# Kernel optimization log

Measured on AMD Instinct MI355X. Metric: run time of the kernel, lower is better.

## Reference

```python
import jax, jax.numpy as jnp
import numpy as np


def _gru(xs, w_ih, w_hh, b_ih, b_hh):
    """Batch-first torch-style GRU. xs: (B,T,I) -> (B,T,H)."""
    b, t, _ = xs.shape
    H = w_hh.shape[1]
    xp = xs @ w_ih.T + b_ih  # (B,T,3H): precomputed input projections

    def step(h, xp_t):
        gh = h @ w_hh.T + b_hh  # (B,3H)
        xr, xz, xn = xp_t[:, :H], xp_t[:, H:2 * H], xp_t[:, 2 * H:]
        hr, hz, hn = gh[:, :H], gh[:, H:2 * H], gh[:, 2 * H:]
        r = jax.nn.sigmoid(xr + hr)
        z = jax.nn.sigmoid(xz + hz)
        n = jnp.tanh(xn + r * hn)
        h_new = (1.0 - z) * n + z * h
        return h_new, h_new

    h0 = jnp.zeros((b, H), dtype=xs.dtype)
    _, hs = jax.lax.scan(step, h0, jnp.swapaxes(xp, 0, 1))  # (T,B,H)
    return jnp.swapaxes(hs, 0, 1)


def reference(x, gru_w_ih, gru_w_hh, gru_b_ih, gru_b_hh, filter_alpha, pc_w, pc_b, pat_re, pat_im):
    b, t, _ = x.shape
    xs = x[..., 0]  # (B,T)
    # quaternionic lift: (w,x,y,z) = (s, .1s, .01s, .001s)
    quat = jnp.stack([xs, 0.1 * xs, 0.01 * xs, 0.001 * xs], axis=-1)  # (B,T,4)
    evolved = _gru(quat, gru_w_ih, gru_w_hh, gru_b_ih, gru_b_hh)  # (B,T,4*dim)
    dim2 = evolved.shape[-1] // 2
    ev = evolved.reshape(b, t, dim2, 2)
    ec = jax.lax.complex(ev[..., 0], ev[..., 1])  # (B,T,2*dim) complex64
    fd = jnp.fft.fft(ec, axis=1)
    kmag = jnp.abs(fd) + 1e-10
    pf = filter_alpha[0] * jnp.arctan(jnp.log(kmag))  # phase filter
    filtered = fd * jax.lax.complex(jnp.cos(pf), jnp.sin(pf))
    ft = jnp.fft.ifft(filtered, axis=1).real  # (B,T,2*dim) float32
    coh = ft.reshape(b, t, -1) @ pc_w.T + pc_b  # (B,T,dim)
    # interference logits: |<x_t, pattern_j>|^2, computed only for batch 0
    # (faithful to original; x_t is real so vdot conjugation is a no-op)
    x0 = coh[0]  # (T,dim)
    zr = x0 @ pat_re.T  # (T,V)
    zi = x0 @ pat_im.T  # (T,V)
    logits0 = zr * zr + zi * zi
    return logits0[None]  # (1,T,V)


def setup_inputs() -> dict:
    key = jax.random.key(0)
    ks = jax.random.split(key, 10)
    dim, T, V = 128, 4096, 32000
    H = dim * 4
    return {
        "x": jax.random.normal(ks[0], (1, T, 1), jnp.float32),
        "gru_w_ih": jax.random.normal(ks[1], (3 * H, 4), jnp.float32) * 0.05,
        "gru_w_hh": jax.random.normal(ks[2], (3 * H, H), jnp.float32) * 0.05,
        "gru_b_ih": jax.random.normal(ks[3], (3 * H,), jnp.float32) * 0.05,
        "gru_b_hh": jax.random.normal(ks[4], (3 * H,), jnp.float32) * 0.05,
        "filter_alpha": jnp.ones((1,), jnp.float32) * 1.5,
        "pc_w": jax.random.normal(ks[5], (dim, 2 * dim), jnp.float32) * 0.05,
        "pc_b": jax.random.normal(ks[6], (dim,), jnp.float32) * 0.05,
        "pat_re": jax.random.normal(ks[7], (V, dim), jnp.float32) * 0.1,
        "pat_im": jax.random.normal(ks[8], (V, dim), jnp.float32) * 0.1,
    }
```

## Files before the change

kernel.cpp:

```cpp
#include <hip/hip_runtime.h>

#define T_STEPS 4096
#define HID     512
#define NCH     256
#define DIM     128
#define VOCAB   32000
#define GRU_WGS 16

__device__ __forceinline__ float fast_sigmoid(float x) {
  x = fminf(fmaxf(x, -30.f), 30.f);
  const float e = __expf(-x);
  return __fdividef(1.f, 1.f + e);
}
__device__ __forceinline__ float fast_tanh(float x) {
  x = fminf(fmaxf(x, -15.f), 15.f);
  const float e = __expf(2.f * x);
  return __fdividef(e - 1.f, e + 1.f);
}

template <int CTRL>
__device__ __forceinline__ float dpp_add(float v) {
  const int s = __builtin_amdgcn_update_dpp(0, __float_as_int(v), CTRL, 0xF, 0xF, true);
  return v + __int_as_float(s);
}
__device__ __forceinline__ float red16(float v) {
  v = dpp_add<0xB1>(v);
  v = dpp_add<0x4E>(v);
  v = dpp_add<0x124>(v);
  v = dpp_add<0x128>(v);
  return v;
}

__global__ __launch_bounds__(512) void gru_kernel(
    const float* __restrict__ x,
    const float* __restrict__ w_ih,
    const float* __restrict__ w_hh,
    const float* __restrict__ b_ih,
    const float* __restrict__ b_hh,
    unsigned long long* hg,
    float* __restrict__ evolved)
{
  __shared__ float hs[HID];
  __shared__ float xl[T_STEPS];
  const int tid  = threadIdx.x;
  const int wave = tid >> 6;
  const int lane = tid & 63;
  const int team = lane >> 4;
  const int p    = lane & 15;
  const int pr   = p & 7;
  const int j    = blockIdx.x * 32 + wave * 4 + team;
  const int k0   = p * 32;

  {
    const float4* x4 = reinterpret_cast<const float4*>(x);
    float4* xl4 = reinterpret_cast<float4*>(xl);
    for (int u = tid; u < T_STEPS / 4; u += 512) xl4[u] = x4[u];
  }

  float4 w[3][8];
#pragma unroll
  for (int d = 0; d < 3; ++d) {
    const float4* wr = reinterpret_cast<const float4*>(w_hh + (size_t)(d * HID + j) * HID);
#pragma unroll
    for (int qq = 0; qq < 8; ++qq) {
      const int r = (qq + pr) & 7;
      w[d][qq] = wr[p * 8 + r];
    }
  }
  float c3[3], bi3[3], bh3[3];
#pragma unroll
  for (int d = 0; d < 3; ++d) {
    int r = d * HID + j;
    c3[d]  = w_ih[r*4+0] + 0.1f*w_ih[r*4+1] + 0.01f*w_ih[r*4+2] + 0.001f*w_ih[r*4+3];
    bi3[d] = b_ih[r];
    bh3[d] = b_hh[r];
  }
  __syncthreads();

  float hprev = 0.0f;
  for (int s = 1; s <= T_STEPS; ++s) {
    const int rb = (s - 1) & 1;
    const int wb = s & 1;
    const unsigned int want = (unsigned int)(s - 1);
    const unsigned long long* rs = hg + rb * HID;

    const float xt = xl[s - 1];

    unsigned long long v =
        __hip_atomic_load(rs + tid, __ATOMIC_RELAXED, __HIP_MEMORY_SCOPE_AGENT);
    for (;;) {
      hs[tid] = __uint_as_float((unsigned int)v);
      const unsigned long long nv =
          __hip_atomic_load(rs + tid, __ATOMIC_RELAXED, __HIP_MEMORY_SCOPE_AGENT);
      if (__syncthreads_and((unsigned int)(v >> 32) == want)) break;
      v = nv;
    }

    float a0 = 0.f, a1 = 0.f, a2 = 0.f;
#pragma unroll
    for (int qq = 0; qq < 8; ++qq) {
      const int r = (qq + pr) & 7;
      const float4 h4 = *reinterpret_cast<const float4*>(&hs[k0 + 4 * r]);
      a0 = fmaf(w[0][qq].x, h4.x, a0);
      a0 = fmaf(w[0][qq].y, h4.y, a0);
      a0 = fmaf(w[0][qq].z, h4.z, a0);
      a0 = fmaf(w[0][qq].w, h4.w, a0);
      a1 = fmaf(w[1][qq].x, h4.x, a1);
      a1 = fmaf(w[1][qq].y, h4.y, a1);
      a1 = fmaf(w[1][qq].z, h4.z, a1);
      a1 = fmaf(w[1][qq].w, h4.w, a1);
      a2 = fmaf(w[2][qq].x, h4.x, a2);
      a2 = fmaf(w[2][qq].y, h4.y, a2);
      a2 = fmaf(w[2][qq].z, h4.z, a2);
      a2 = fmaf(w[2][qq].w, h4.w, a2);
    }

    a0 = red16(a0); a1 = red16(a1); a2 = red16(a2);

    if (p == 0) {
      const float rg = fast_sigmoid(fmaf(xt, c3[0], bi3[0]) + a0 + bh3[0]);
      const float zg = fast_sigmoid(fmaf(xt, c3[1], bi3[1]) + a1 + bh3[1]);
      const float ng = fast_tanh(fmaf(xt, c3[2], bi3[2]) + rg * (a2 + bh3[2]));
      const float hn = (1.0f - zg) * ng + zg * hprev;
      hprev = hn;
      const unsigned long long pk =
          ((unsigned long long)(unsigned int)s << 32) | (unsigned long long)__float_as_uint(hn);
      __hip_atomic_store(hg + wb * HID + j, pk, __ATOMIC_RELAXED, __HIP_MEMORY_SCOPE_AGENT);
      evolved[(size_t)(s - 1) * HID + j] = hn;
    }
  }
}

__device__ __forceinline__ void fft4096(float2* buf, const float2* tw, int tid)
{
  for (int st = 0; st < 12; ++st) {
    const int half = 1 << st;
    const int sh = 11 - st;
    for (int i = tid; i < 2048; i += 256) {
      const int blk = i >> st;
      const int pos = i & (half - 1);
      const int idx = blk * (2 << st) + pos;
      const float2 t = tw[pos << sh];
      const float2 u = buf[idx];
      const float2 v = buf[idx + half];
      const float tr = v.x * t.x - v.y * t.y;
      const float ti = v.x * t.y + v.y * t.x;
      buf[idx]        = make_float2(u.x + tr, u.y + ti);
      buf[idx + half] = make_float2(u.x - tr, u.y - ti);
    }
    __syncthreads();
  }
}

__global__ __launch_bounds__(256) void fft_kernel(
    const float* __restrict__ evolved,
    const float* __restrict__ alpha_p,
    float* __restrict__ ft)
{
  __shared__ float2 buf[4096];
  __shared__ float2 tw[2048];
  const int tid = threadIdx.x;
  const int c = blockIdx.x;
  const float alpha = alpha_p[0];

  for (int k = tid; k < 2048; k += 256) {
    float sn, cs;
    sincosf(-6.283185307179586f * (float)k / 4096.0f, &sn, &cs);
    tw[k] = make_float2(cs, sn);
  }

  for (int t = tid; t < 4096; t += 256) {
    const int r = __brev((unsigned)t) >> 20;
    buf[r] = make_float2(evolved[(size_t)t * HID + 2 * c],
                         evolved[(size_t)t * HID + 2 * c + 1]);
  }
  __syncthreads();
  fft4096(buf, tw, tid);

  for (int t = tid; t < 4096; t += 256) {
    float2 v = buf[t];
    const float km = sqrtf(v.x * v.x + v.y * v.y) + 1e-10f;
    const float pf = alpha * atanf(logf(km));
    float sn, cs;
    sincosf(pf, &sn, &cs);
    const float rr = v.x * cs - v.y * sn;
    const float ii = v.x * sn + v.y * cs;
    buf[t] = make_float2(rr, -ii);
  }
  __syncthreads();
  for (int t = tid; t < 4096; t += 256) {
    const int r = __brev((unsigned)t) >> 20;
    if (r > t) { float2 tmp = buf[t]; buf[t] = buf[r]; buf[r] = tmp; }
  }
  __syncthreads();
  fft4096(buf, tw, tid);

  const float inv = 1.0f / 4096.0f;
  for (int t = tid; t < 4096; t += 256) {
    ft[(size_t)t * NCH + c] = buf[t].x * inv;
  }
}

__global__ __launch_bounds__(256) void coh_kernel(
    const float* __restrict__ ft,
    const float* __restrict__ pcw,
    const float* __restrict__ pcb,
    float* __restrict__ x0)
{
  __shared__ float wT[64][132];
  __shared__ float fT[64][68];
  const int tid = threadIdx.x;
  const int rg = tid >> 4;
  const int cg = tid & 15;
  const int t0 = blockIdx.x * 64;
  float acc[4][8];
#pragma unroll
  for (int i = 0; i < 4; ++i)
#pragma unroll
    for (int jj = 0; jj < 8; ++jj) acc[i][jj] = 0.f;

  for (int kt = 0; kt < 256; kt += 64) {
    __syncthreads();
    for (int u = tid; u < 64 * DIM; u += 256) {
      const int col = u >> 6, kk = u & 63;
      wT[kk][col] = pcw[col * 256 + kt + kk];
    }
    for (int u = tid; u < 64 * 64; u += 256) {
      const int row = u >> 6, kk = u & 63;
      fT[kk][row] = ft[(size_t)(t0 + row) * NCH + kt + kk];
    }
    __syncthreads();
#pragma unroll 4
    for (int k = 0; k < 64; ++k) {
      const float4 a  = *(const float4*)&fT[k][rg * 4];
      const float4 w0 = *(const float4*)&wT[k][cg * 8];
      const float4 w1 = *(const float4*)&wT[k][cg * 8 + 4];
      const float av[4] = {a.x, a.y, a.z, a.w};
      const float wv[8] = {w0.x, w0.y, w0.z, w0.w, w1.x, w1.y, w1.z, w1.w};
#pragma unroll
      for (int i = 0; i < 4; ++i)
#pragma unroll
        for (int jj = 0; jj < 8; ++jj)
          acc[i][jj] = fmaf(av[i], wv[jj], acc[i][jj]);
    }
  }
#pragma unroll
  for (int i = 0; i < 4; ++i) {
    const int t = t0 + rg * 4 + i;
#pragma unroll
    for (int jj = 0; jj < 8; ++jj)
      x0[(size_t)t * DIM + cg * 8 + jj] = acc[i][jj] + pcb[cg * 8 + jj];
  }
}

__global__ __launch_bounds__(256) void logits_kernel(
    const float* __restrict__ x0,
    const float* __restrict__ patre,
    const float* __restrict__ patim,
    float* __restrict__ out)
{
  __shared__ float aT[32][68];
  __shared__ float brT[32][132];
  __shared__ float biT[32][132];
  const int tid = threadIdx.x;
  const int tx = tid & 31;
  const int ty = tid >> 5;
  const int m0 = blockIdx.y * 64;
  const int n0 = blockIdx.x * 128;
  float accr[8][4], acci[8][4];
#pragma unroll
  for (int i = 0; i < 8; ++i)
#pragma unroll
    for (int jj = 0; jj < 4; ++jj) { accr[i][jj] = 0.f; acci[i][jj] = 0.f; }

  for (int kt = 0; kt < 128; kt += 32) {
    __syncthreads();
    for (int u = tid; u < 64 * 32; u += 256) {
      const int mm = u >> 5, kk = u & 31;
      aT[kk][mm] = x0[(size_t)(m0 + mm) * DIM + kt + kk];
    }
    for (int u = tid; u < 128 * 32; u += 256) {
      const int nn = u >> 5, kk = u & 31;
      brT[kk][nn] = patre[(size_t)(n0 + nn) * DIM + kt + kk];
      biT[kk][nn] = patim[(size_t)(n0 + nn) * DIM + kt + kk];
    }
    __syncthreads();
#pragma unroll 4
    for (int k = 0; k < 32; ++k) {
      const float4 q0 = *(const float4*)&aT[k][ty * 8];
      const float4 q1 = *(const float4*)&aT[k][ty * 8 + 4];
      const float4 br = *(const float4*)&brT[k][tx * 4];
      const float4 bi = *(const float4*)&biT[k][tx * 4];
      const float av[8]  = {q0.x, q0.y, q0.z, q0.w, q1.x, q1.y, q1.z, q1.w};
      const float brv[4] = {br.x, br.y, br.z, br.w};
      const float biv[4] = {bi.x, bi.y, bi.z, bi.w};
#pragma unroll
      for (int i = 0; i < 8; ++i)
#pragma unroll
        for (int jj = 0; jj < 4; ++jj) {
          accr[i][jj] = fmaf(av[i], brv[jj], accr[i][jj]);
          acci[i][jj] = fmaf(av[i], biv[jj], acci[i][jj]);
        }
    }
  }
#pragma unroll
  for (int i = 0; i < 8; ++i) {
    const size_t m = (size_t)(m0 + ty * 8 + i);
    float4 o;
    o.x = accr[i][0] * accr[i][0] + acci[i][0] * acci[i][0];
    o.y = accr[i][1] * accr[i][1] + acci[i][1] * acci[i][1];
    o.z = accr[i][2] * accr[i][2] + acci[i][2] * acci[i][2];
    o.w = accr[i][3] * accr[i][3] + acci[i][3] * acci[i][3];
    *(float4*)&out[m * VOCAB + n0 + tx * 4] = o;
  }
}

extern "C" void kernel_launch(void* const* d_in, const int* in_sizes, int n_in,
                              void* d_out, int out_size, void* d_ws, size_t ws_size,
                              hipStream_t stream)
{
  const float* x     = (const float*)d_in[0];
  const float* w_ih  = (const float*)d_in[1];
  const float* w_hh  = (const float*)d_in[2];
  const float* b_ih  = (const float*)d_in[3];
  const float* b_hh  = (const float*)d_in[4];
  const float* alpha = (const float*)d_in[5];
  const float* pc_w  = (const float*)d_in[6];
  const float* pc_b  = (const float*)d_in[7];
  const float* patre = (const float*)d_in[8];
  const float* patim = (const float*)d_in[9];

  float* out = (float*)d_out;
  float* evolved = out;
  float* ft      = out + 4194304;

  unsigned long long* hg = (unsigned long long*)d_ws;
  float* x0 = (float*)((char*)d_ws + 16384);

  hipMemsetAsync(d_ws, 0, 8192, stream);

  gru_kernel<<<GRU_WGS, 512, 0, stream>>>(x, w_ih, w_hh, b_ih, b_hh, hg, evolved);
  fft_kernel<<<256, 256, 0, stream>>>(evolved, alpha, ft);
  coh_kernel<<<64, 256, 0, stream>>>(ft, pc_w, pc_b, x0);
  logits_kernel<<<dim3(250, 64), 256, 0, stream>>>(x0, patre, patim, out);
}
```

Baseline: 10.44 ms.

## Replicate GRU hidden-state mailboxes per workgroup and switch FFT to radix-4

Each GRU workgroup now polls its own private copy of the hidden-state exchange buffer, and every producer writes its value into all 16 copies. This is meant to cut contention on the shared polled cache lines in the serial recurrence, at the cost of 16 times more atomic stores per step. Separately, the FFT moves from radix-2 to radix-4 butterflies with digit-reversal ordering and a full twiddle table, halving the number of barrier-separated stages. The workspace memset and the x0 offset grow to fit the larger mailbox area.

```diff
diff --git a/kernel.cpp b/kernel.cpp
--- a/kernel.cpp
+++ b/kernel.cpp
@@ -50,6 +50,7 @@
   const int pr   = p & 7;
   const int j    = blockIdx.x * 32 + wave * 4 + team;
   const int k0   = p * 32;
+  unsigned long long* mybox = hg + (size_t)blockIdx.x * 1024;
 
   {
     const float4* x4 = reinterpret_cast<const float4*>(x);
@@ -82,7 +83,7 @@
     const int rb = (s - 1) & 1;
     const int wb = s & 1;
     const unsigned int want = (unsigned int)(s - 1);
-    const unsigned long long* rs = hg + rb * HID;
+    const unsigned long long* rs = mybox + rb * HID;
 
     const float xt = xl[s - 1];
 
@@ -125,31 +126,54 @@
       hprev = hn;
       const unsigned long long pk =
           ((unsigned long long)(unsigned int)s << 32) | (unsigned long long)__float_as_uint(hn);
-      __hip_atomic_store(hg + wb * HID + j, pk, __ATOMIC_RELAXED, __HIP_MEMORY_SCOPE_AGENT);
+      unsigned long long* dst = hg + (size_t)wb * HID + j;
+#pragma unroll
+      for (int wgt = 0; wgt < GRU_WGS; ++wgt)
+        __hip_atomic_store(dst + wgt * 1024, pk, __ATOMIC_RELAXED, __HIP_MEMORY_SCOPE_AGENT);
       evolved[(size_t)(s - 1) * HID + j] = hn;
     }
   }
 }
 
-__device__ __forceinline__ void fft4096(float2* buf, const float2* tw, int tid)
-{
-  for (int st = 0; st < 12; ++st) {
-    const int half = 1 << st;
-    const int sh = 11 - st;
-    for (int i = tid; i < 2048; i += 256) {
-      const int blk = i >> st;
-      const int pos = i & (half - 1);
-      const int idx = blk * (2 << st) + pos;
-      const float2 t = tw[pos << sh];
-      const float2 u = buf[idx];
-      const float2 v = buf[idx + half];
-      const float tr = v.x * t.x - v.y * t.y;
-      const float ti = v.x * t.y + v.y * t.x;
-      buf[idx]        = make_float2(u.x + tr, u.y + ti);
-      buf[idx + half] = make_float2(u.x - tr, u.y - ti);
-    }
-    __syncthreads();
-  }
+__device__ __forceinline__ float2 cmul(float2 a, float2 b) {
+  return make_float2(a.x * b.x - a.y * b.y, a.x * b.y + a.y * b.x);
+}
+
+__device__ __forceinline__ void fft4096_r4(float2* buf, const float2* tw, int tid)
+{
+  for (int st = 0; st < 6; ++st) {
+    const int q  = 1 << (2 * st);
+    const int ts = 10 - 2 * st;
+    for (int i = tid; i < 1024; i += 256) {
+      const int blk  = i >> (2 * st);
+      const int pos  = i & (q - 1);
+      const int base = blk * (q << 2) + pos;
+      const float2 u0 = buf[base];
+      float2 u1 = buf[base + q];
+      float2 u2 = buf[base + 2 * q];
+      float2 u3 = buf[base + 3 * q];
+      const int k = pos << ts;
+      u1 = cmul(u1, tw[k]);
+      u2 = cmul(u2, tw[2 * k]);
+      u3 = cmul(u3, tw[3 * k]);
+      const float ax = u0.x + u2.x, ay = u0.y + u2.y;
+      const float bx = u0.x - u2.x, by = u0.y - u2.y;
+      const float cx = u1.x + u3.x, cy = u1.y + u3.y;
+      const float dx = u1.x - u3.x, dy = u1.y - u3.y;
+      buf[base]         = make_float2(ax + cx, ay + cy);
+      buf[base + q]     = make_float2(bx + dy, by - dx);
+      buf[base + 2 * q] = make_float2(ax - cx, ay - cy);
+      buf[base + 3 * q] = make_float2(bx - dy, by + dx);
+    }
+    __syncthreads();
+  }
+}
+
+__device__ __forceinline__ int digitrev4(int t) {
+  int r = 0;
+#pragma unroll
+  for (int d = 0; d < 6; ++d) { r = (r << 2) | (t & 3); t >>= 2; }
+  return r;
 }
 
 __global__ __launch_bounds__(256) void fft_kernel(
@@ -158,24 +182,23 @@
     float* __restrict__ ft)
 {
   __shared__ float2 buf[4096];
-  __shared__ float2 tw[2048];
+  __shared__ float2 tw[4096];
   const int tid = threadIdx.x;
   const int c = blockIdx.x;
   const float alpha = alpha_p[0];
 
-  for (int k = tid; k < 2048; k += 256) {
+  for (int k = tid; k < 4096; k += 256) {
     float sn, cs;
     sincosf(-6.283185307179586f * (float)k / 4096.0f, &sn, &cs);
     tw[k] = make_float2(cs, sn);
   }
 
   for (int t = tid; t < 4096; t += 256) {
-    const int r = __brev((unsigned)t) >> 20;
-    buf[r] = make_float2(evolved[(size_t)t * HID + 2 * c],
-                         evolved[(size_t)t * HID + 2 * c + 1]);
+    buf[digitrev4(t)] = make_float2(evolved[(size_t)t * HID + 2 * c],
+                                    evolved[(size_t)t * HID + 2 * c + 1]);
   }
   __syncthreads();
-  fft4096(buf, tw, tid);
+  fft4096_r4(buf, tw, tid);
 
   for (int t = tid; t < 4096; t += 256) {
     float2 v = buf[t];
@@ -189,11 +212,11 @@
   }
   __syncthreads();
   for (int t = tid; t < 4096; t += 256) {
-    const int r = __brev((unsigned)t) >> 20;
+    const int r = digitrev4(t);
     if (r > t) { float2 tmp = buf[t]; buf[t] = buf[r]; buf[r] = tmp; }
   }
   __syncthreads();
-  fft4096(buf, tw, tid);
+  fft4096_r4(buf, tw, tid);
 
   const float inv = 1.0f / 4096.0f;
   for (int t = tid; t < 4096; t += 256) {
@@ -335,9 +358,9 @@
   float* ft      = out + 4194304;
 
   unsigned long long* hg = (unsigned long long*)d_ws;
-  float* x0 = (float*)((char*)d_ws + 16384);
-
-  hipMemsetAsync(d_ws, 0, 8192, stream);
+  float* x0 = (float*)((char*)d_ws + 131072);
+
+  hipMemsetAsync(d_ws, 0, 131072, stream);
 
   gru_kernel<<<GRU_WGS, 512, 0, stream>>>(x, w_ih, w_hh, b_ih, b_hh, hg, evolved);
   fft_kernel<<<256, 256, 0, stream>>>(evolved, alpha, ft);
```

Measured after the change: 12.54 ms. 20.1% more time.
